# Kernel tuning notes

Hardware: AMD Instinct MI355X
Metric: run time of the kernel (lower is better)

Reference implementation:

```python
import jax, jax.numpy as jnp
import numpy as np

B, S, H, T = 32, 4096, 1024, 512

def setup_inputs() -> dict:
    key = jax.random.key(0)
    ks = jax.random.split(key, 6)
    scale = 1.0 / np.sqrt(H)
    return {
        "x": jax.random.normal(ks[0], (B, H), jnp.float32),
        "context": jax.random.normal(ks[1], (B, S, H), jnp.float32),
        "topic": jax.random.normal(ks[2], (B, T), jnp.float32),
        "W_in": jax.random.normal(ks[3], (H, H), jnp.float32) * scale,
        "b_in": jnp.zeros((H,), jnp.float32),
        "W_out": jax.random.normal(ks[4], (H, 2 * H + T), jnp.float32) * scale,
        "b_out": jnp.zeros((H,), jnp.float32),
    }

def reference(x, context, topic, W_in, b_in, W_out, b_out):
    # gamma_h = linear_in(x): [B, H]  (activation=None -> no tanh here)
    gamma = x @ W_in.T + b_in
    # scores = bmm(context, gamma_h.unsqueeze(2)).squeeze(2): [B, S]
    scores = jnp.einsum('bsh,bh->bs', context, gamma)
    weights = jax.nn.softmax(scores, axis=-1)
    # c_t = bmm(weights.unsqueeze(1), context).squeeze(1): [B, H]
    c_t = jnp.einsum('bs,bsh->bh', weights, context)
    cat = jnp.concatenate([c_t, x, topic], axis=1)  # [B, 2H+T]
    output = jnp.tanh(cat @ W_out.T + b_out)  # [B, H]
    return (output, weights)
```

## Files before the change

kernel.cpp:

```cpp
#include <hip/hip_runtime.h>
#include <math.h>

#define B_ 32
#define S_ 4096
#define H_ 1024
#define T_ 512
#define OUTK_ (2*H_ + T_)

__global__ __launch_bounds__(256) void k_gamma(const float* __restrict__ x,
                                               const float* __restrict__ W_in,
                                               const float* __restrict__ b_in,
                                               float* __restrict__ gamma) {
    int lane = threadIdx.x & 63;
    int wid  = blockIdx.x * 4 + (threadIdx.x >> 6);
    int i    = wid >> 1;
    int b0   = (wid & 1) * 16;
    const float4* Wr = (const float4*)(W_in + (size_t)i * H_);
    float4 wf[4];
    #pragma unroll
    for (int k = 0; k < 4; ++k) wf[k] = Wr[k*64 + lane];
    float bias = b_in[i];
    for (int bb = 0; bb < 16; ++bb) {
        int b = b0 + bb;
        const float4* xr = (const float4*)(x + (size_t)b * H_);
        float p = 0.f;
        #pragma unroll
        for (int k = 0; k < 4; ++k) {
            float4 v = xr[k*64 + lane];
            p += v.x*wf[k].x + v.y*wf[k].y + v.z*wf[k].z + v.w*wf[k].w;
        }
        #pragma unroll
        for (int off = 32; off >= 1; off >>= 1) p += __shfl_xor(p, off, 64);
        if (lane == 0) gamma[(size_t)b * H_ + i] = p + bias;
    }
}

__global__ __launch_bounds__(256) void k_scores_online(const float* __restrict__ context,
                                                       const float* __restrict__ gamma,
                                                       float* __restrict__ scores,
                                                       float* __restrict__ pm,
                                                       float* __restrict__ pl,
                                                       float* __restrict__ pacc,
                                                       int WPB, int rows) {
    int lane = threadIdx.x & 63;
    int b    = blockIdx.y;
    int wave = blockIdx.x * 4 + (threadIdx.x >> 6);

    const float4* gr = (const float4*)(gamma + (size_t)b * H_);
    float4 g[4];
    #pragma unroll
    for (int k = 0; k < 4; ++k) g[k] = gr[k*64 + lane];

    const float4* ctx = (const float4*)(context + (size_t)b * S_ * H_);
    float  m = -INFINITY, l = 0.f;
    float4 acc[4];
    #pragma unroll
    for (int k = 0; k < 4; ++k) acc[k] = make_float4(0.f, 0.f, 0.f, 0.f);

    int s0 = wave * rows;
    for (int s = s0; s < s0 + rows; ++s) {
        float4 c[4];
        #pragma unroll
        for (int k = 0; k < 4; ++k) c[k] = ctx[(size_t)s*256 + k*64 + lane];
        float p = 0.f;
        #pragma unroll
        for (int k = 0; k < 4; ++k)
            p += c[k].x*g[k].x + c[k].y*g[k].y + c[k].z*g[k].z + c[k].w*g[k].w;
        #pragma unroll
        for (int off = 32; off >= 1; off >>= 1) p += __shfl_xor(p, off, 64);
        if (lane == 0) scores[(size_t)b*S_ + s] = p;

        float mnew  = fmaxf(m, p);
        float scale = __expf(m - mnew);
        float w     = __expf(p - mnew);
        l = l * scale + w;
        #pragma unroll
        for (int k = 0; k < 4; ++k) {
            acc[k].x = acc[k].x*scale + w*c[k].x;
            acc[k].y = acc[k].y*scale + w*c[k].y;
            acc[k].z = acc[k].z*scale + w*c[k].z;
            acc[k].w = acc[k].w*scale + w*c[k].w;
        }
        m = mnew;
    }

    int pw = b * WPB + wave;
    if (lane == 0) { pm[pw] = m; pl[pw] = l; }
    float4* pa = (float4*)(pacc + (size_t)pw * H_);
    #pragma unroll
    for (int k = 0; k < 4; ++k) pa[k*64 + lane] = acc[k];
}

__global__ __launch_bounds__(256) void k_ct(const float* __restrict__ pm,
                                            const float* __restrict__ pl,
                                            const float* __restrict__ pacc,
                                            float* __restrict__ ct,
                                            int WPB) {
    __shared__ float red[128];
    __shared__ float ew[128];
    int tid = threadIdx.x;
    int b   = blockIdx.y;

    float mv = -INFINITY;
    if (tid < WPB) mv = pm[b*WPB + tid];
    if (tid < 128) red[tid] = mv;
    __syncthreads();
    for (int st = 64; st >= 1; st >>= 1) {
        if (tid < st) red[tid] = fmaxf(red[tid], red[tid + st]);
        __syncthreads();
    }
    float M = red[0];
    __syncthreads();

    float term = 0.f;
    if (tid < WPB) {
        float e = __expf(pm[b*WPB + tid] - M);
        ew[tid] = e;
        term = pl[b*WPB + tid] * e;
    }
    if (tid < 128) red[tid] = term;
    __syncthreads();
    for (int st = 64; st >= 1; st >>= 1) {
        if (tid < st) red[tid] += red[tid + st];
        __syncthreads();
    }
    float invL = 1.f / red[0];

    int h = blockIdx.x * 256 + tid;
    float c = 0.f;
    for (int w = 0; w < WPB; ++w)
        c += ew[w] * pacc[(size_t)(b*WPB + w) * H_ + h];
    ct[(size_t)b*H_ + h] = c * invL;
}

__global__ __launch_bounds__(256) void k_weights(const float* __restrict__ pm,
                                                 const float* __restrict__ pl,
                                                 const float* __restrict__ scores,
                                                 float* __restrict__ wout,
                                                 int WPB) {
    __shared__ float red[128];
    int tid = threadIdx.x;
    int b   = blockIdx.y;

    float mv = -INFINITY;
    if (tid < WPB) mv = pm[b*WPB + tid];
    if (tid < 128) red[tid] = mv;
    __syncthreads();
    for (int st = 64; st >= 1; st >>= 1) {
        if (tid < st) red[tid] = fmaxf(red[tid], red[tid + st]);
        __syncthreads();
    }
    float M = red[0];
    __syncthreads();

    float term = (tid < WPB) ? pl[b*WPB + tid] * __expf(pm[b*WPB + tid] - M) : 0.f;
    if (tid < 128) red[tid] = term;
    __syncthreads();
    for (int st = 64; st >= 1; st >>= 1) {
        if (tid < st) red[tid] += red[tid + st];
        __syncthreads();
    }
    float invL = 1.f / red[0];

    int s = blockIdx.x * 256 + tid;
    wout[(size_t)b*S_ + s] = __expf(scores[(size_t)b*S_ + s] - M) * invL;
}

__global__ __launch_bounds__(256) void k_out(const float* __restrict__ ct,
                                             const float* __restrict__ x,
                                             const float* __restrict__ topic,
                                             const float* __restrict__ W_out,
                                             const float* __restrict__ b_out,
                                             float* __restrict__ out) {
    int lane = threadIdx.x & 63;
    int wid  = blockIdx.x * 4 + (threadIdx.x >> 6);
    int i    = wid >> 1;
    int b0   = (wid & 1) * 16;
    const float4* Wr = (const float4*)(W_out + (size_t)i * OUTK_);
    float4 wf[10];
    #pragma unroll
    for (int k = 0; k < 10; ++k) wf[k] = Wr[k*64 + lane];
    float bias = b_out[i];
    for (int bb = 0; bb < 16; ++bb) {
        int b = b0 + bb;
        const float4* cr = (const float4*)(ct    + (size_t)b*H_);
        const float4* xr = (const float4*)(x     + (size_t)b*H_);
        const float4* tr = (const float4*)(topic + (size_t)b*T_);
        float p = 0.f;
        #pragma unroll
        for (int k = 0; k < 4; ++k) {
            float4 v = cr[k*64 + lane];
            p += v.x*wf[k].x + v.y*wf[k].y + v.z*wf[k].z + v.w*wf[k].w;
        }
        #pragma unroll
        for (int k = 0; k < 4; ++k) {
            float4 v = xr[k*64 + lane];
            p += v.x*wf[4+k].x + v.y*wf[4+k].y + v.z*wf[4+k].z + v.w*wf[4+k].w;
        }
        #pragma unroll
        for (int k = 0; k < 2; ++k) {
            float4 v = tr[k*64 + lane];
            p += v.x*wf[8+k].x + v.y*wf[8+k].y + v.z*wf[8+k].z + v.w*wf[8+k].w;
        }
        #pragma unroll
        for (int off = 32; off >= 1; off >>= 1) p += __shfl_xor(p, off, 64);
        if (lane == 0) out[(size_t)b*H_ + i] = tanhf(p + bias);
    }
}

extern "C" void kernel_launch(void* const* d_in, const int* in_sizes, int n_in,
                              void* d_out, int out_size, void* d_ws, size_t ws_size,
                              hipStream_t stream) {
    const float* x       = (const float*)d_in[0];
    const float* context = (const float*)d_in[1];
    const float* topic   = (const float*)d_in[2];
    const float* W_in    = (const float*)d_in[3];
    const float* b_in    = (const float*)d_in[4];
    const float* W_out   = (const float*)d_in[5];
    const float* b_out   = (const float*)d_in[6];

    float* out     = (float*)d_out;
    float* weights = out + (size_t)B_ * H_;

    int WPB = 128;
    while (WPB > 4) {
        size_t need = ((size_t)(B_*H_ + B_*S_ + B_*H_) +
                       (size_t)B_ * WPB * (2 + H_)) * sizeof(float);
        if (need <= ws_size) break;
        WPB >>= 1;
    }
    int rows = S_ / WPB;

    float* ws     = (float*)d_ws;
    float* gamma  = ws;
    float* scores = gamma  + (size_t)B_ * H_;
    float* ct     = scores + (size_t)B_ * S_;
    float* pm     = ct     + (size_t)B_ * H_;
    float* pl     = pm     + (size_t)B_ * WPB;
    float* pacc   = pl     + (size_t)B_ * WPB;

    hipLaunchKernelGGL(k_gamma, dim3(512), dim3(256), 0, stream,
                       x, W_in, b_in, gamma);
    hipLaunchKernelGGL(k_scores_online, dim3(WPB/4, B_), dim3(256), 0, stream,
                       context, gamma, scores, pm, pl, pacc, WPB, rows);
    hipLaunchKernelGGL(k_ct, dim3(H_/256, B_), dim3(256), 0, stream,
                       pm, pl, pacc, ct, WPB);
    hipLaunchKernelGGL(k_weights, dim3(S_/256, B_), dim3(256), 0, stream,
                       pm, pl, scores, weights, WPB);
    hipLaunchKernelGGL(k_out, dim3(512), dim3(256), 0, stream,
                       ct, x, topic, W_out, b_out, out);
}
```

Measured before the change: 760.8 us.

## Unroll online-softmax loop by two rows and merge ct/weights finalize kernels

The scores kernel now processes two context rows per iteration, issuing both rows' loads together for more memory-level parallelism and doing one max/rescale per pair. The ct and weights kernels are merged into a single finalize launch that splits blocks by index. WPB becomes a compile-time constant of 128, which removes the workspace-size fallback and fixes the loop trip count. The cost is higher register pressure from holding twice the context data, and a hard dependency on the workspace being large enough.

Result: no change. 759.4 us (-0.2%).

```diff
diff --git a/kernel.cpp b/kernel.cpp
--- a/kernel.cpp
+++ b/kernel.cpp
@@ -6,6 +6,8 @@
 #define H_ 1024
 #define T_ 512
 #define OUTK_ (2*H_ + T_)
+#define WPB_ 128
+#define ROWS_ (S_ / WPB_)
 
 __global__ __launch_bounds__(256) void k_gamma(const float* __restrict__ x,
                                                const float* __restrict__ W_in,
@@ -40,8 +42,7 @@
                                                        float* __restrict__ scores,
                                                        float* __restrict__ pm,
                                                        float* __restrict__ pl,
-                                                       float* __restrict__ pacc,
-                                                       int WPB, int rows) {
+                                                       float* __restrict__ pacc) {
     int lane = threadIdx.x & 63;
     int b    = blockIdx.y;
     int wave = blockIdx.x * 4 + (threadIdx.x >> 6);
@@ -57,52 +58,64 @@
     #pragma unroll
     for (int k = 0; k < 4; ++k) acc[k] = make_float4(0.f, 0.f, 0.f, 0.f);
 
-    int s0 = wave * rows;
-    for (int s = s0; s < s0 + rows; ++s) {
-        float4 c[4];
-        #pragma unroll
-        for (int k = 0; k < 4; ++k) c[k] = ctx[(size_t)s*256 + k*64 + lane];
-        float p = 0.f;
-        #pragma unroll
-        for (int k = 0; k < 4; ++k)
-            p += c[k].x*g[k].x + c[k].y*g[k].y + c[k].z*g[k].z + c[k].w*g[k].w;
-        #pragma unroll
-        for (int off = 32; off >= 1; off >>= 1) p += __shfl_xor(p, off, 64);
-        if (lane == 0) scores[(size_t)b*S_ + s] = p;
-
-        float mnew  = fmaxf(m, p);
-        float scale = __expf(m - mnew);
-        float w     = __expf(p - mnew);
-        l = l * scale + w;
-        #pragma unroll
-        for (int k = 0; k < 4; ++k) {
-            acc[k].x = acc[k].x*scale + w*c[k].x;
-            acc[k].y = acc[k].y*scale + w*c[k].y;
-            acc[k].z = acc[k].z*scale + w*c[k].z;
-            acc[k].w = acc[k].w*scale + w*c[k].w;
+    int s0 = wave * ROWS_;
+    for (int s = s0; s < s0 + ROWS_; s += 2) {
+        float4 c0[4], c1[4];
+        #pragma unroll
+        for (int k = 0; k < 4; ++k) c0[k] = ctx[(size_t)s*256 + k*64 + lane];
+        #pragma unroll
+        for (int k = 0; k < 4; ++k) c1[k] = ctx[(size_t)(s+1)*256 + k*64 + lane];
+
+        float p0 = 0.f, p1 = 0.f;
+        #pragma unroll
+        for (int k = 0; k < 4; ++k) {
+            p0 += c0[k].x*g[k].x + c0[k].y*g[k].y + c0[k].z*g[k].z + c0[k].w*g[k].w;
+            p1 += c1[k].x*g[k].x + c1[k].y*g[k].y + c1[k].z*g[k].z + c1[k].w*g[k].w;
+        }
+        #pragma unroll
+        for (int off = 32; off >= 1; off >>= 1) {
+            p0 += __shfl_xor(p0, off, 64);
+            p1 += __shfl_xor(p1, off, 64);
+        }
+        if (lane == 0) {
+            scores[(size_t)b*S_ + s]     = p0;
+            scores[(size_t)b*S_ + s + 1] = p1;
+        }
+
+        float mnew  = fmaxf(m, fmaxf(p0, p1));
+        float scale = __expf(m  - mnew);
+        float w0    = __expf(p0 - mnew);
+        float w1    = __expf(p1 - mnew);
+        l = l * scale + w0 + w1;
+        #pragma unroll
+        for (int k = 0; k < 4; ++k) {
+            acc[k].x = acc[k].x*scale + w0*c0[k].x + w1*c1[k].x;
+            acc[k].y = acc[k].y*scale + w0*c0[k].y + w1*c1[k].y;
+            acc[k].z = acc[k].z*scale + w0*c0[k].z + w1*c1[k].z;
+            acc[k].w = acc[k].w*scale + w0*c0[k].w + w1*c1[k].w;
         }
         m = mnew;
     }
 
-    int pw = b * WPB + wave;
+    int pw = b * WPB_ + wave;
     if (lane == 0) { pm[pw] = m; pl[pw] = l; }
     float4* pa = (float4*)(pacc + (size_t)pw * H_);
     #pragma unroll
     for (int k = 0; k < 4; ++k) pa[k*64 + lane] = acc[k];
 }
 
-__global__ __launch_bounds__(256) void k_ct(const float* __restrict__ pm,
-                                            const float* __restrict__ pl,
-                                            const float* __restrict__ pacc,
-                                            float* __restrict__ ct,
-                                            int WPB) {
+__global__ __launch_bounds__(256) void k_finalize(const float* __restrict__ pm,
+                                                  const float* __restrict__ pl,
+                                                  const float* __restrict__ pacc,
+                                                  const float* __restrict__ scores,
+                                                  float* __restrict__ ct,
+                                                  float* __restrict__ wout) {
     __shared__ float red[128];
-    __shared__ float ew[128];
+    __shared__ float ew[WPB_];
     int tid = threadIdx.x;
     int b   = blockIdx.y;
 
-    float mv = -INFINITY;
-    if (tid < WPB) mv = pm[b*WPB + tid];
+    float mv = (tid < WPB_) ? pm[b*WPB_ + tid] : -INFINITY;
     if (tid < 128) red[tid] = mv;
     __syncthreads();
     for (int st = 64; st >= 1; st >>= 1) {
@@ -113,10 +126,10 @@
     __syncthreads();
 
     float term = 0.f;
-    if (tid < WPB) {
-        float e = __expf(pm[b*WPB + tid] - M);
+    if (tid < WPB_) {
+        float e = __expf(pm[b*WPB_ + tid] - M);
         ew[tid] = e;
-        term = pl[b*WPB + tid] * e;
+        term = pl[b*WPB_ + tid] * e;
     }
     if (tid < 128) red[tid] = term;
     __syncthreads();
@@ -126,44 +139,16 @@
     }
     float invL = 1.f / red[0];
 
-    int h = blockIdx.x * 256 + tid;
-    float c = 0.f;
-    for (int w = 0; w < WPB; ++w)
-        c += ew[w] * pacc[(size_t)(b*WPB + w) * H_ + h];
-    ct[(size_t)b*H_ + h] = c * invL;
-}
-
-__global__ __launch_bounds__(256) void k_weights(const float* __restrict__ pm,
-                                                 const float* __restrict__ pl,
-                                                 const float* __restrict__ scores,
-                                                 float* __restrict__ wout,
-                                                 int WPB) {
-    __shared__ float red[128];
-    int tid = threadIdx.x;
-    int b   = blockIdx.y;
-
-    float mv = -INFINITY;
-    if (tid < WPB) mv = pm[b*WPB + tid];
-    if (tid < 128) red[tid] = mv;
-    __syncthreads();
-    for (int st = 64; st >= 1; st >>= 1) {
-        if (tid < st) red[tid] = fmaxf(red[tid], red[tid + st]);
-        __syncthreads();
-    }
-    float M = red[0];
-    __syncthreads();
-
-    float term = (tid < WPB) ? pl[b*WPB + tid] * __expf(pm[b*WPB + tid] - M) : 0.f;
-    if (tid < 128) red[tid] = term;
-    __syncthreads();
-    for (int st = 64; st >= 1; st >>= 1) {
-        if (tid < st) red[tid] += red[tid + st];
-        __syncthreads();
-    }
-    float invL = 1.f / red[0];
-
-    int s = blockIdx.x * 256 + tid;
-    wout[(size_t)b*S_ + s] = __expf(scores[(size_t)b*S_ + s] - M) * invL;
+    if (blockIdx.x < H_/256) {
+        int h = blockIdx.x * 256 + tid;
+        float c = 0.f;
+        for (int w = 0; w < WPB_; ++w)
+            c += ew[w] * pacc[(size_t)(b*WPB_ + w) * H_ + h];
+        ct[(size_t)b*H_ + h] = c * invL;
+    } else {
+        int s = (blockIdx.x - H_/256) * 256 + tid;
+        wout[(size_t)b*S_ + s] = __expf(scores[(size_t)b*S_ + s] - M) * invL;
+    }
 }
 
 __global__ __launch_bounds__(256) void k_out(const float* __restrict__ ct,
@@ -222,31 +207,20 @@
     float* out     = (float*)d_out;
     float* weights = out + (size_t)B_ * H_;
 
-    int WPB = 128;
-    while (WPB > 4) {
-        size_t need = ((size_t)(B_*H_ + B_*S_ + B_*H_) +
-                       (size_t)B_ * WPB * (2 + H_)) * sizeof(float);
-        if (need <= ws_size) break;
-        WPB >>= 1;
-    }
-    int rows = S_ / WPB;
-
     float* ws     = (float*)d_ws;
     float* gamma  = ws;
     float* scores = gamma  + (size_t)B_ * H_;
     float* ct     = scores + (size_t)B_ * S_;
     float* pm     = ct     + (size_t)B_ * H_;
-    float* pl     = pm     + (size_t)B_ * WPB;
-    float* pacc   = pl     + (size_t)B_ * WPB;
+    float* pl     = pm     + (size_t)B_ * WPB_;
+    float* pacc   = pl     + (size_t)B_ * WPB_;
 
     hipLaunchKernelGGL(k_gamma, dim3(512), dim3(256), 0, stream,
                        x, W_in, b_in, gamma);
-    hipLaunchKernelGGL(k_scores_online, dim3(WPB/4, B_), dim3(256), 0, stream,
-                       context, gamma, scores, pm, pl, pacc, WPB, rows);
-    hipLaunchKernelGGL(k_ct, dim3(H_/256, B_), dim3(256), 0, stream,
-                       pm, pl, pacc, ct, WPB);
-    hipLaunchKernelGGL(k_weights, dim3(S_/256, B_), dim3(256), 0, stream,
-                       pm, pl, scores, weights, WPB);
+    hipLaunchKernelGGL(k_scores_online, dim3(WPB_/4, B_), dim3(256), 0, stream,
+                       context, gamma, scores, pm, pl, pacc);
+    hipLaunchKernelGGL(k_finalize, dim3(H_/256 + S_/256, B_), dim3(256), 0, stream,
+                       pm, pl, pacc, scores, ct, weights);
     hipLaunchKernelGGL(k_out, dim3(512), dim3(256), 0, stream,
                        ct, x, topic, W_out, b_out, out);
 }
```
